# Kernel optimization log

Hardware: AMD Instinct MI355X
Metric: run time of the kernel (lower is better)

## Reference

```python
import jax, jax.numpy as jnp
import numpy as np

D_MODEL = 1024
NUM_HEADS = 16
D_K = D_MODEL // NUM_HEADS
THETA = 10000.0
BATCH = 4
SEQ = 2048


def rope(x, positions, theta=THETA):
    # x: [B, H, S, d_k]; rotate interleaved pairs (x_{2i}, x_{2i+1})
    d_k = x.shape[-1]
    inv_freq = theta ** (-jnp.arange(0, d_k, 2, dtype=jnp.float32) / d_k)  # [d_k/2]
    ang = positions[:, None].astype(jnp.float32) * inv_freq[None, :]  # [S, d_k/2]
    cos, sin = jnp.cos(ang), jnp.sin(ang)
    x1 = x[..., 0::2]
    x2 = x[..., 1::2]
    r1 = x1 * cos - x2 * sin
    r2 = x1 * sin + x2 * cos
    out = jnp.stack([r1, r2], axis=-1).reshape(x.shape)
    return out.astype(x.dtype)


def setup_inputs() -> dict:
    key = jax.random.key(0)
    k0, k1, k2, k3, k4 = jax.random.split(key, 5)
    std_qk = 2.0 / (D_MODEL + D_MODEL)
    x = jax.random.normal(k0, (BATCH, SEQ, D_MODEL), dtype=jnp.float32)
    P_Q = jax.random.normal(k1, (D_MODEL, D_MODEL), dtype=jnp.float32) * std_qk
    P_K = jax.random.normal(k2, (D_MODEL, D_MODEL), dtype=jnp.float32) * std_qk
    P_V = jax.random.normal(k3, (D_MODEL, D_MODEL), dtype=jnp.float32) * std_qk
    P_O = jax.random.normal(k4, (D_MODEL, D_MODEL), dtype=jnp.float32) * std_qk
    return {"x": x, "P_Q": P_Q, "P_K": P_K, "P_V": P_V, "P_O": P_O}


def reference(x, P_Q, P_K, P_V, P_O):
    B, S, _ = x.shape
    positions = jnp.arange(S)

    def proj(P):
        y = jnp.einsum('bsd,ed->bse', x, P)  # e = num_heads*d_k
        return y.reshape(B, S, NUM_HEADS, D_K).transpose(0, 2, 1, 3)  # [B,H,S,d_k]

    Q = rope(proj(P_Q), positions)
    K = rope(proj(P_K), positions)
    V = proj(P_V)

    scores = jnp.einsum('bhqd,bhkd->bhqk', Q, K) / jnp.sqrt(jnp.asarray(D_K, x.dtype))
    causal = jnp.tril(jnp.ones((S, S), dtype=bool))
    scores = jnp.where(causal, scores, jnp.asarray(-jnp.inf, scores.dtype))
    attn = jax.nn.softmax(scores, axis=-1)
    out = jnp.einsum('bhqk,bhkd->bhqd', attn, V)  # [B,H,S,d_v]
    out = out.transpose(0, 2, 1, 3).reshape(B, S, NUM_HEADS * D_K)
    return jnp.einsum('bse,de->bsd', out, P_O)
```

## Files before the change

kernel.cpp:

```cpp
#include <hip/hip_runtime.h>

typedef unsigned short u16;
typedef unsigned int u32;
typedef float f32x4 __attribute__((ext_vector_type(4)));
typedef __bf16 bf16x8 __attribute__((ext_vector_type(8)));

#define S_LEN 2048
#define DMODEL 1024
#define NHEAD 16
#define DKH 64

__device__ __forceinline__ u16 f2bf(float f) {
    unsigned u = __float_as_uint(f);
    u += 0x7FFFu + ((u >> 16) & 1u);
    return (u16)(u >> 16);
}
__device__ __forceinline__ u32 pk2(float a, float b) {
    return (u32)f2bf(a) | ((u32)f2bf(b) << 16);
}

__device__ __forceinline__ void glds16(const u16* g, u16* l) {
    __builtin_amdgcn_global_load_lds(
        (const __attribute__((address_space(1))) void*)(g),
        (__attribute__((address_space(3))) void*)(l), 16, 0, 0);
}

__global__ __launch_bounds__(256) void cvt_kernel(const float* __restrict__ in,
                                                  u16* __restrict__ out, int n4) {
    int i = blockIdx.x * 256 + threadIdx.x;
    if (i >= n4) return;
    float4 v = reinterpret_cast<const float4*>(in)[i];
    uint2 o;
    o.x = (unsigned)f2bf(v.x) | ((unsigned)f2bf(v.y) << 16);
    o.y = (unsigned)f2bf(v.z) | ((unsigned)f2bf(v.w) << 16);
    reinterpret_cast<uint2*>(out)[i] = o;
}

__device__ __forceinline__ void gemm_core(const u16* __restrict__ A, const u16* __restrict__ Bt,
                                          int K, int m0, int n0,
                                          u16* As, u16* Bs, f32x4 acc[4][4]) {
    const int tid  = threadIdx.x;
    const int lane = tid & 63;
    const int quad = lane >> 4, l15 = lane & 15;
    const int w    = tid >> 6;
    const int mq   = w & 1, nq = w >> 1;

    const int c0 = tid, c1 = tid + 256;
    const int r0 = c0 >> 2, k0 = ((c0 & 3) ^ (r0 & 3)) * 8;
    const int r1 = c1 >> 2, k1 = ((c1 & 3) ^ (r1 & 3)) * 8;
    const u16* ga0 = A  + (size_t)(m0 + r0) * K + k0;
    const u16* ga1 = A  + (size_t)(m0 + r1) * K + k1;
    const u16* gb0 = Bt + (size_t)(n0 + r0) * K + k0;
    const u16* gb1 = Bt + (size_t)(n0 + r1) * K + k1;
    u16* la0 = As + c0 * 8; u16* la1 = As + c1 * 8;
    u16* lb0 = Bs + c0 * 8; u16* lb1 = Bs + c1 * 8;

    const int swz = (quad ^ (l15 & 3)) * 8;
    const u16* ra = As + (mq * 64 + l15) * 32 + swz;
    const u16* rb = Bs + (nq * 64 + l15) * 32 + swz;

    for (int kk = 0; kk < K; kk += 32) {
        __syncthreads();
        glds16(ga0 + kk, la0);
        glds16(ga1 + kk, la1);
        glds16(gb0 + kk, lb0);
        glds16(gb1 + kk, lb1);
        __syncthreads();
        bf16x8 af[4], bfv[4];
#pragma unroll
        for (int t = 0; t < 4; ++t) {
            af[t]  = *reinterpret_cast<const bf16x8*>(ra + t * 512);
            bfv[t] = *reinterpret_cast<const bf16x8*>(rb + t * 512);
        }
#pragma unroll
        for (int mt = 0; mt < 4; ++mt)
#pragma unroll
            for (int nt = 0; nt < 4; ++nt)
                acc[mt][nt] = __builtin_amdgcn_mfma_f32_16x16x32_bf16(af[mt], bfv[nt], acc[mt][nt], 0, 0, 0);
    }
}

__global__ __launch_bounds__(256) void gemm_qkv_kernel(const u16* __restrict__ xb, const u16* __restrict__ Wqkv,
                                                       u16* __restrict__ Qb, u16* __restrict__ Kb,
                                                       u16* __restrict__ Vt) {
    __shared__ u16 As[128 * 32];
    __shared__ u16 Bs[128 * 32];
    f32x4 acc[4][4];
    const f32x4 zz = {0.f, 0.f, 0.f, 0.f};
#pragma unroll
    for (int i = 0; i < 4; ++i)
#pragma unroll
        for (int j = 0; j < 4; ++j) acc[i][j] = zz;

    const int m0 = blockIdx.y * 128;
    const int n0 = blockIdx.x * 128;
    gemm_core(xb, Wqkv, DMODEL, m0, n0, As, Bs, acc);

    const int lane = threadIdx.x & 63;
    const int quad = lane >> 4, l15 = lane & 15;
    const int w = threadIdx.x >> 6, mq = w & 1, nq = w >> 1;

#pragma unroll
    for (int nt = 0; nt < 4; ++nt) {
        const int ncol = n0 + nq*64 + nt*16 + l15;
        const int sel  = ncol >> 10;
        const int e    = ncol & 1023;
        const int h    = e >> 6, dk = e & 63;
#pragma unroll
        for (int mt = 0; mt < 4; ++mt) {
            const int mrow = m0 + mq*64 + mt*16 + quad*4;
            if (sel == 2) {
#pragma unroll
                for (int r = 0; r < 4; ++r) {
                    int m = mrow + r;
                    int b = m >> 11, s = m & 2047;
                    Vt[((size_t)(b * NHEAD + h) * DKH + dk) * S_LEN + s] = f2bf(acc[mt][nt][r]);
                }
            } else {
                float invf = exp2f(-13.2877124f * (float)(dk & 62) * (1.0f / 64.0f));
                u16* dst = sel ? Kb : Qb;
#pragma unroll
                for (int r = 0; r < 4; ++r) {
                    float val  = acc[mt][nt][r];
                    float part = __shfl_xor(val, 1);
                    int m = mrow + r;
                    int b = m >> 11, s = m & 2047;
                    float ang = (float)s * invf;
                    float sn, cs;
                    __sincosf(ang, &sn, &cs);
                    float o = (dk & 1) ? (part * sn + val * cs)
                                       : (val * cs - part * sn);
                    dst[((size_t)(b * NHEAD + h) * S_LEN + s) * DKH + dk] = f2bf(o);
                }
            }
        }
    }
}

__global__ __launch_bounds__(256) void attn_kernel(const u16* __restrict__ Qb, const u16* __restrict__ Kb,
                                                   const u16* __restrict__ Vt, u16* __restrict__ A2) {
    __shared__ u16 Ks[64 * 64];
    __shared__ u16 Vs[64 * 64];
    __shared__ u16 Ps[4][32 * 64];

    const int tid  = threadIdx.x;
    const int lane = tid & 63, w = tid >> 6;
    const int quad = lane >> 4, l15 = lane & 15;
    const int bh   = blockIdx.x & 63;
    const int qb   = 15 - (blockIdx.x >> 6);
    const int b = bh >> 4, h = bh & 15;
    const int q0w = qb * 128 + w * 32;
    const int nkt = 2 * (qb + 1);
    const int sw7 = l15 & 7;
    const float csc = 0.125f * 1.44269504f;
    const f32x4 zz = {0.f, 0.f, 0.f, 0.f};

    bf16x8 qf[2][2];
#pragma unroll
    for (int qt2 = 0; qt2 < 2; ++qt2)
#pragma unroll
        for (int hh = 0; hh < 2; ++hh)
            qf[qt2][hh] = *reinterpret_cast<const bf16x8*>(
                Qb + ((size_t)bh * S_LEN + q0w + qt2 * 16 + l15) * DKH + hh * 32 + quad * 8);

    f32x4 st[4][2], ot[4][2];
#pragma unroll
    for (int mt = 0; mt < 4; ++mt) { ot[mt][0] = zz; ot[mt][1] = zz; }
    float mi[2] = {-3.0e38f, -3.0e38f}, li[2] = {0.f, 0.f};

    const int c0 = tid, c1 = tid + 256;
    const int r0 = c0 >> 3, kc0 = ((c0 & 7) ^ (r0 & 7)) * 8;
    const int r1 = c1 >> 3, kc1 = ((c1 & 7) ^ (r1 & 7)) * 8;
    const u16* gk0 = Kb + ((size_t)bh * S_LEN + r0) * DKH + kc0;
    const u16* gk1 = Kb + ((size_t)bh * S_LEN + r1) * DKH + kc1;
    const u16* gv0 = Vt + ((size_t)bh * DKH + r0) * S_LEN + kc0;
    const u16* gv1 = Vt + ((size_t)bh * DKH + r1) * S_LEN + kc1;
    u16* lk0 = Ks + c0 * 8; u16* lk1 = Ks + c1 * 8;
    u16* lv0 = Vs + c0 * 8; u16* lv1 = Vs + c1 * 8;
    u16* Pw = &Ps[w][0];

    for (int kt = 0; kt < nkt; ++kt) {
        const int key0 = kt * 64;
        __syncthreads();
        glds16(gk0 + (size_t)key0 * DKH, lk0);
        glds16(gk1 + (size_t)key0 * DKH, lk1);
        glds16(gv0 + key0, lv0);
        glds16(gv1 + key0, lv1);
        __syncthreads();

#pragma unroll
        for (int kt4 = 0; kt4 < 4; ++kt4) {
            const u16* krow = Ks + (kt4 * 16 + l15) * 64;
            bf16x8 ka0 = *reinterpret_cast<const bf16x8*>(krow + (quad ^ sw7) * 8);
            bf16x8 ka1 = *reinterpret_cast<const bf16x8*>(krow + ((4 + quad) ^ sw7) * 8);
#pragma unroll
            for (int qt2 = 0; qt2 < 2; ++qt2) {
                f32x4 s = __builtin_amdgcn_mfma_f32_16x16x32_bf16(ka0, qf[qt2][0], zz, 0, 0, 0);
                st[kt4][qt2] = __builtin_amdgcn_mfma_f32_16x16x32_bf16(ka1, qf[qt2][1], s, 0, 0, 0);
            }
        }

        if (key0 + 63 > q0w) {
#pragma unroll
            for (int qt2 = 0; qt2 < 2; ++qt2) {
                const int qrow = q0w + qt2 * 16 + l15;
#pragma unroll
                for (int kt4 = 0; kt4 < 4; ++kt4) {
                    const int kbase = key0 + kt4 * 16 + quad * 4;
#pragma unroll
                    for (int r = 0; r < 4; ++r)
                        if (kbase + r > qrow) st[kt4][qt2][r] = -3.0e38f;
                }
            }
        }

#pragma unroll
        for (int qt2 = 0; qt2 < 2; ++qt2) {
            float rm = st[0][qt2][0];
#pragma unroll
            for (int kt4 = 0; kt4 < 4; ++kt4)
#pragma unroll
                for (int r = 0; r < 4; ++r) rm = fmaxf(rm, st[kt4][qt2][r]);
            rm = fmaxf(rm, __shfl_xor(rm, 16));
            rm = fmaxf(rm, __shfl_xor(rm, 32));
            const float mn = fmaxf(mi[qt2], rm);
            const float al = exp2f((mi[qt2] - mn) * csc);
            mi[qt2] = mn;
            const float nb = mn * csc;
            float rs = 0.f;
#pragma unroll
            for (int kt4 = 0; kt4 < 4; ++kt4)
#pragma unroll
                for (int r = 0; r < 4; ++r) {
                    float p = exp2f(st[kt4][qt2][r] * csc - nb);
                    st[kt4][qt2][r] = p;
                    rs += p;
                }
            rs += __shfl_xor(rs, 16);
            rs += __shfl_xor(rs, 32);
            li[qt2] = li[qt2] * al + rs;
#pragma unroll
            for (int mt = 0; mt < 4; ++mt)
#pragma unroll
                for (int r = 0; r < 4; ++r) ot[mt][qt2][r] *= al;

            u16* prow = Pw + (qt2 * 16 + l15) * 64 + (quad & 1) * 4;
#pragma unroll
            for (int kt4 = 0; kt4 < 4; ++kt4) {
                uint2 pv;
                pv.x = pk2(st[kt4][qt2][0], st[kt4][qt2][1]);
                pv.y = pk2(st[kt4][qt2][2], st[kt4][qt2][3]);
                *reinterpret_cast<uint2*>(prow + ((2 * kt4 + (quad >> 1)) ^ sw7) * 8) = pv;
            }
        }
        __threadfence_block();

        bf16x8 pb[2][2];
#pragma unroll
        for (int qt2 = 0; qt2 < 2; ++qt2)
#pragma unroll
            for (int kh = 0; kh < 2; ++kh)
                pb[qt2][kh] = *reinterpret_cast<const bf16x8*>(
                    Pw + (qt2 * 16 + l15) * 64 + ((kh * 4 + quad) ^ sw7) * 8);
#pragma unroll
        for (int mt = 0; mt < 4; ++mt) {
            const u16* vrow = Vs + (mt * 16 + l15) * 64;
            bf16x8 va0 = *reinterpret_cast<const bf16x8*>(vrow + (quad ^ sw7) * 8);
            bf16x8 va1 = *reinterpret_cast<const bf16x8*>(vrow + ((4 + quad) ^ sw7) * 8);
#pragma unroll
            for (int qt2 = 0; qt2 < 2; ++qt2) {
                ot[mt][qt2] = __builtin_amdgcn_mfma_f32_16x16x32_bf16(va0, pb[qt2][0], ot[mt][qt2], 0, 0, 0);
                ot[mt][qt2] = __builtin_amdgcn_mfma_f32_16x16x32_bf16(va1, pb[qt2][1], ot[mt][qt2], 0, 0, 0);
            }
        }
    }

#pragma unroll
    for (int qt2 = 0; qt2 < 2; ++qt2) {
        const float il = 1.0f / li[qt2];
        u16* prow = Pw + (qt2 * 16 + l15) * 64 + (quad & 1) * 4;
#pragma unroll
        for (int mt = 0; mt < 4; ++mt) {
            uint2 ov;
            ov.x = pk2(ot[mt][qt2][0] * il, ot[mt][qt2][1] * il);
            ov.y = pk2(ot[mt][qt2][2] * il, ot[mt][qt2][3] * il);
            *reinterpret_cast<uint2*>(prow + ((2 * mt + (quad >> 1)) ^ sw7) * 8) = ov;
        }
    }
    __threadfence_block();
    const int r2 = lane >> 1, half = lane & 1;
    const u16* orow = Pw + r2 * 64;
    u16* gout = A2 + ((size_t)b * S_LEN + q0w + r2) * DMODEL + h * DKH + half * 32;
#pragma unroll
    for (int c = 0; c < 4; ++c) {
        uint4 val = *reinterpret_cast<const uint4*>(orow + (((half * 4 + c) ^ (r2 & 7))) * 8);
        *reinterpret_cast<uint4*>(gout + c * 8) = val;
    }
}

__global__ __launch_bounds__(256) void gemm_oproj_kernel(const u16* __restrict__ A2, const u16* __restrict__ Wo,
                                                         float* __restrict__ Cout) {
    __shared__ u16 As[128 * 32];
    __shared__ u16 Bs[128 * 32];
    f32x4 acc[4][4];
    const f32x4 zz = {0.f, 0.f, 0.f, 0.f};
#pragma unroll
    for (int i = 0; i < 4; ++i)
#pragma unroll
        for (int j = 0; j < 4; ++j) acc[i][j] = zz;

    const int m0 = blockIdx.y * 128;
    const int n0 = blockIdx.x * 128;
    gemm_core(A2, Wo, DMODEL, m0, n0, As, Bs, acc);

    const int lane = threadIdx.x & 63;
    const int quad = lane >> 4, l15 = lane & 15;
    const int w = threadIdx.x >> 6, mq = w & 1, nq = w >> 1;
#pragma unroll
    for (int nt = 0; nt < 4; ++nt) {
        const int ncol = n0 + nq*64 + nt*16 + l15;
#pragma unroll
        for (int mt = 0; mt < 4; ++mt) {
            const int mrow = m0 + mq*64 + mt*16 + quad*4;
#pragma unroll
            for (int r = 0; r < 4; ++r)
                Cout[(size_t)(mrow + r) * DMODEL + ncol] = acc[mt][nt][r];
        }
    }
}

extern "C" void kernel_launch(void* const* d_in, const int* in_sizes, int n_in,
                              void* d_out, int out_size, void* d_ws, size_t ws_size,
                              hipStream_t stream) {
    const float* x  = (const float*)d_in[0];
    const float* PQ = (const float*)d_in[1];
    const float* PK = (const float*)d_in[2];
    const float* PV = (const float*)d_in[3];
    const float* PO = (const float*)d_in[4];
    float* out = (float*)d_out;
    char* ws = (char*)d_ws;

    const size_t MB = 1u << 20;
    u16* xb   = (u16*)(ws + 0 * MB);
    u16* Wqkv = (u16*)(ws + 16 * MB);
    u16* Wo   = (u16*)(ws + 22 * MB);
    u16* Qb   = (u16*)(ws + 24 * MB);
    u16* Kb   = (u16*)(ws + 40 * MB);
    u16* Vt   = (u16*)(ws + 56 * MB);
    u16* A2   = (u16*)(ws + 72 * MB);

    cvt_kernel<<<dim3(8192), dim3(256), 0, stream>>>(x,  xb,            2097152);
    cvt_kernel<<<dim3(1024), dim3(256), 0, stream>>>(PQ, Wqkv,           262144);
    cvt_kernel<<<dim3(1024), dim3(256), 0, stream>>>(PK, Wqkv + 1048576, 262144);
    cvt_kernel<<<dim3(1024), dim3(256), 0, stream>>>(PV, Wqkv + 2097152, 262144);
    cvt_kernel<<<dim3(1024), dim3(256), 0, stream>>>(PO, Wo,             262144);

    gemm_qkv_kernel<<<dim3(24, 64), dim3(256), 0, stream>>>(xb, Wqkv, Qb, Kb, Vt);

    attn_kernel<<<dim3(1024), dim3(256), 0, stream>>>(Qb, Kb, Vt, A2);

    gemm_oproj_kernel<<<dim3(8, 64), dim3(256), 0, stream>>>(A2, Wo, out);
}
```

Measured before the change: 314.3 us.

## Double-buffer K/V tiles, pair causal query blocks, and cheapen softmax/RoPE math

The attention kernel now double-buffers the K/V shared-memory tiles and issues the next tile's async load before computing on the current one, so global loads overlap with MFMA work. Each workgroup processes a short and a long causal query block in turn, which balances work across the halved grid. The online softmax skips the rescale of the output accumulator when no row maximum grew, bf16 packing uses the hardware packed-convert builtin, and RoPE uses range-reduced native sin/cos. These trade extra LDS and some rounding and sin/cos accuracy differences for less load latency and fewer ALU instructions.

```diff
diff --git a/kernel.cpp b/kernel.cpp
--- a/kernel.cpp
+++ b/kernel.cpp
@@ -15,8 +15,15 @@
     u += 0x7FFFu + ((u >> 16) & 1u);
     return (u16)(u >> 16);
 }
-__device__ __forceinline__ u32 pk2(float a, float b) {
+
+__device__ __forceinline__ u32 pkbf2(float a, float b) {
+#if __has_builtin(__builtin_amdgcn_cvt_pk_bf16_f32)
+    typedef __bf16 bf16x2_t __attribute__((ext_vector_type(2)));
+    bf16x2_t r = __builtin_amdgcn_cvt_pk_bf16_f32(a, b);
+    u32 u; __builtin_memcpy(&u, &r, 4); return u;
+#else
     return (u32)f2bf(a) | ((u32)f2bf(b) << 16);
+#endif
 }
 
 __device__ __forceinline__ void glds16(const u16* g, u16* l) {
@@ -117,7 +124,7 @@
                     Vt[((size_t)(b * NHEAD + h) * DKH + dk) * S_LEN + s] = f2bf(acc[mt][nt][r]);
                 }
             } else {
-                float invf = exp2f(-13.2877124f * (float)(dk & 62) * (1.0f / 64.0f));
+                float invf_rev = 0.15915494f * exp2f(-13.2877124f * (float)(dk & 62) * (1.0f / 64.0f));
                 u16* dst = sel ? Kb : Qb;
 #pragma unroll
                 for (int r = 0; r < 4; ++r) {
@@ -125,9 +132,15 @@
                     float part = __shfl_xor(val, 1);
                     int m = mrow + r;
                     int b = m >> 11, s = m & 2047;
-                    float ang = (float)s * invf;
+                    float rev = (float)s * invf_rev;
+                    float fr  = rev - floorf(rev);
+#if __has_builtin(__builtin_amdgcn_sinf) && __has_builtin(__builtin_amdgcn_cosf)
+                    float sn = __builtin_amdgcn_sinf(fr);
+                    float cs = __builtin_amdgcn_cosf(fr);
+#else
                     float sn, cs;
-                    __sincosf(ang, &sn, &cs);
+                    __sincosf(fr * 6.2831853f, &sn, &cs);
+#endif
                     float o = (dk & 1) ? (part * sn + val * cs)
                                        : (val * cs - part * sn);
                     dst[((size_t)(b * NHEAD + h) * S_LEN + s) * DKH + dk] = f2bf(o);
@@ -139,34 +152,19 @@
 
 __global__ __launch_bounds__(256) void attn_kernel(const u16* __restrict__ Qb, const u16* __restrict__ Kb,
                                                    const u16* __restrict__ Vt, u16* __restrict__ A2) {
-    __shared__ u16 Ks[64 * 64];
-    __shared__ u16 Vs[64 * 64];
+    __shared__ u16 Ks[2][64 * 64];
+    __shared__ u16 Vs[2][64 * 64];
     __shared__ u16 Ps[4][32 * 64];
 
     const int tid  = threadIdx.x;
     const int lane = tid & 63, w = tid >> 6;
     const int quad = lane >> 4, l15 = lane & 15;
     const int bh   = blockIdx.x & 63;
-    const int qb   = 15 - (blockIdx.x >> 6);
+    const int pr   = blockIdx.x >> 6;
     const int b = bh >> 4, h = bh & 15;
-    const int q0w = qb * 128 + w * 32;
-    const int nkt = 2 * (qb + 1);
     const int sw7 = l15 & 7;
     const float csc = 0.125f * 1.44269504f;
     const f32x4 zz = {0.f, 0.f, 0.f, 0.f};
-
-    bf16x8 qf[2][2];
-#pragma unroll
-    for (int qt2 = 0; qt2 < 2; ++qt2)
-#pragma unroll
-        for (int hh = 0; hh < 2; ++hh)
-            qf[qt2][hh] = *reinterpret_cast<const bf16x8*>(
-                Qb + ((size_t)bh * S_LEN + q0w + qt2 * 16 + l15) * DKH + hh * 32 + quad * 8);
-
-    f32x4 st[4][2], ot[4][2];
-#pragma unroll
-    for (int mt = 0; mt < 4; ++mt) { ot[mt][0] = zz; ot[mt][1] = zz; }
-    float mi[2] = {-3.0e38f, -3.0e38f}, li[2] = {0.f, 0.f};
 
     const int c0 = tid, c1 = tid + 256;
     const int r0 = c0 >> 3, kc0 = ((c0 & 7) ^ (r0 & 7)) * 8;
@@ -175,126 +173,159 @@
     const u16* gk1 = Kb + ((size_t)bh * S_LEN + r1) * DKH + kc1;
     const u16* gv0 = Vt + ((size_t)bh * DKH + r0) * S_LEN + kc0;
     const u16* gv1 = Vt + ((size_t)bh * DKH + r1) * S_LEN + kc1;
-    u16* lk0 = Ks + c0 * 8; u16* lk1 = Ks + c1 * 8;
-    u16* lv0 = Vs + c0 * 8; u16* lv1 = Vs + c1 * 8;
     u16* Pw = &Ps[w][0];
 
-    for (int kt = 0; kt < nkt; ++kt) {
-        const int key0 = kt * 64;
+#pragma unroll 1
+    for (int ph = 0; ph < 2; ++ph) {
+        const int qb  = ph ? (15 - pr) : pr;
+        const int q0w = qb * 128 + w * 32;
+        const int nkt = 2 * (qb + 1);
+
+        bf16x8 qf[2][2];
+#pragma unroll
+        for (int qt2 = 0; qt2 < 2; ++qt2)
+#pragma unroll
+            for (int hh = 0; hh < 2; ++hh)
+                qf[qt2][hh] = *reinterpret_cast<const bf16x8*>(
+                    Qb + ((size_t)bh * S_LEN + q0w + qt2 * 16 + l15) * DKH + hh * 32 + quad * 8);
+
+        f32x4 st[4][2], ot[4][2];
+#pragma unroll
+        for (int mt = 0; mt < 4; ++mt) { ot[mt][0] = zz; ot[mt][1] = zz; }
+        float mi[2] = {-3.0e38f, -3.0e38f}, li[2] = {0.f, 0.f};
+
         __syncthreads();
-        glds16(gk0 + (size_t)key0 * DKH, lk0);
-        glds16(gk1 + (size_t)key0 * DKH, lk1);
-        glds16(gv0 + key0, lv0);
-        glds16(gv1 + key0, lv1);
-        __syncthreads();
-
-#pragma unroll
-        for (int kt4 = 0; kt4 < 4; ++kt4) {
-            const u16* krow = Ks + (kt4 * 16 + l15) * 64;
-            bf16x8 ka0 = *reinterpret_cast<const bf16x8*>(krow + (quad ^ sw7) * 8);
-            bf16x8 ka1 = *reinterpret_cast<const bf16x8*>(krow + ((4 + quad) ^ sw7) * 8);
+        glds16(gk0, &Ks[0][0] + c0 * 8);
+        glds16(gk1, &Ks[0][0] + c1 * 8);
+        glds16(gv0, &Vs[0][0] + c0 * 8);
+        glds16(gv1, &Vs[0][0] + c1 * 8);
+
+#pragma unroll 1
+        for (int kt = 0; kt < nkt; ++kt) {
+            const int key0 = kt * 64;
+            __syncthreads();
+            if (kt + 1 < nkt) {
+                const int nx = (kt + 1) & 1;
+                const size_t nkey = (size_t)(key0 + 64);
+                glds16(gk0 + nkey * DKH, &Ks[nx][0] + c0 * 8);
+                glds16(gk1 + nkey * DKH, &Ks[nx][0] + c1 * 8);
+                glds16(gv0 + nkey, &Vs[nx][0] + c0 * 8);
+                glds16(gv1 + nkey, &Vs[nx][0] + c1 * 8);
+            }
+            const u16* Kbuf = &Ks[kt & 1][0];
+            const u16* Vbuf = &Vs[kt & 1][0];
+
+#pragma unroll
+            for (int kt4 = 0; kt4 < 4; ++kt4) {
+                const u16* krow = Kbuf + (kt4 * 16 + l15) * 64;
+                bf16x8 ka0 = *reinterpret_cast<const bf16x8*>(krow + (quad ^ sw7) * 8);
+                bf16x8 ka1 = *reinterpret_cast<const bf16x8*>(krow + ((4 + quad) ^ sw7) * 8);
+#pragma unroll
+                for (int qt2 = 0; qt2 < 2; ++qt2) {
+                    f32x4 s = __builtin_amdgcn_mfma_f32_16x16x32_bf16(ka0, qf[qt2][0], zz, 0, 0, 0);
+                    st[kt4][qt2] = __builtin_amdgcn_mfma_f32_16x16x32_bf16(ka1, qf[qt2][1], s, 0, 0, 0);
+                }
+            }
+
+            if (key0 + 63 > q0w) {
+#pragma unroll
+                for (int qt2 = 0; qt2 < 2; ++qt2) {
+                    const int qrow = q0w + qt2 * 16 + l15;
+#pragma unroll
+                    for (int kt4 = 0; kt4 < 4; ++kt4) {
+                        const int kbase = key0 + kt4 * 16 + quad * 4;
+#pragma unroll
+                        for (int r = 0; r < 4; ++r)
+                            if (kbase + r > qrow) st[kt4][qt2][r] = -3.0e38f;
+                    }
+                }
+            }
+
 #pragma unroll
             for (int qt2 = 0; qt2 < 2; ++qt2) {
-                f32x4 s = __builtin_amdgcn_mfma_f32_16x16x32_bf16(ka0, qf[qt2][0], zz, 0, 0, 0);
-                st[kt4][qt2] = __builtin_amdgcn_mfma_f32_16x16x32_bf16(ka1, qf[qt2][1], s, 0, 0, 0);
-            }
-        }
-
-        if (key0 + 63 > q0w) {
-#pragma unroll
-            for (int qt2 = 0; qt2 < 2; ++qt2) {
-                const int qrow = q0w + qt2 * 16 + l15;
+                float rm = st[0][qt2][0];
+#pragma unroll
+                for (int kt4 = 0; kt4 < 4; ++kt4)
+#pragma unroll
+                    for (int r = 0; r < 4; ++r) rm = fmaxf(rm, st[kt4][qt2][r]);
+                rm = fmaxf(rm, __shfl_xor(rm, 16));
+                rm = fmaxf(rm, __shfl_xor(rm, 32));
+                if (__ballot(rm > mi[qt2])) {
+                    const float mn = fmaxf(mi[qt2], rm);
+                    const float al = exp2f((mi[qt2] - mn) * csc);
+                    mi[qt2] = mn;
+                    li[qt2] *= al;
+#pragma unroll
+                    for (int mt = 0; mt < 4; ++mt)
+#pragma unroll
+                        for (int r = 0; r < 4; ++r) ot[mt][qt2][r] *= al;
+                }
+                const float nb = mi[qt2] * csc;
+                float rs = 0.f;
+#pragma unroll
+                for (int kt4 = 0; kt4 < 4; ++kt4)
+#pragma unroll
+                    for (int r = 0; r < 4; ++r) {
+                        float p = exp2f(st[kt4][qt2][r] * csc - nb);
+                        st[kt4][qt2][r] = p;
+                        rs += p;
+                    }
+                rs += __shfl_xor(rs, 16);
+                rs += __shfl_xor(rs, 32);
+                li[qt2] += rs;
+
+                u16* prow = Pw + (qt2 * 16 + l15) * 64 + (quad & 1) * 4;
 #pragma unroll
                 for (int kt4 = 0; kt4 < 4; ++kt4) {
-                    const int kbase = key0 + kt4 * 16 + quad * 4;
-#pragma unroll
-                    for (int r = 0; r < 4; ++r)
-                        if (kbase + r > qrow) st[kt4][qt2][r] = -3.0e38f;
+                    uint2 pv;
+                    pv.x = pkbf2(st[kt4][qt2][0], st[kt4][qt2][1]);
+                    pv.y = pkbf2(st[kt4][qt2][2], st[kt4][qt2][3]);
+                    *reinterpret_cast<uint2*>(prow + ((2 * kt4 + (quad >> 1)) ^ sw7) * 8) = pv;
+                }
+            }
+            __threadfence_block();
+
+            bf16x8 pb[2][2];
+#pragma unroll
+            for (int qt2 = 0; qt2 < 2; ++qt2)
+#pragma unroll
+                for (int kh = 0; kh < 2; ++kh)
+                    pb[qt2][kh] = *reinterpret_cast<const bf16x8*>(
+                        Pw + (qt2 * 16 + l15) * 64 + ((kh * 4 + quad) ^ sw7) * 8);
+#pragma unroll
+            for (int mt = 0; mt < 4; ++mt) {
+                const u16* vrow = Vbuf + (mt * 16 + l15) * 64;
+                bf16x8 va0 = *reinterpret_cast<const bf16x8*>(vrow + (quad ^ sw7) * 8);
+                bf16x8 va1 = *reinterpret_cast<const bf16x8*>(vrow + ((4 + quad) ^ sw7) * 8);
+#pragma unroll
+                for (int qt2 = 0; qt2 < 2; ++qt2) {
+                    ot[mt][qt2] = __builtin_amdgcn_mfma_f32_16x16x32_bf16(va0, pb[qt2][0], ot[mt][qt2], 0, 0, 0);
+                    ot[mt][qt2] = __builtin_amdgcn_mfma_f32_16x16x32_bf16(va1, pb[qt2][1], ot[mt][qt2], 0, 0, 0);
                 }
             }
         }
 
 #pragma unroll
         for (int qt2 = 0; qt2 < 2; ++qt2) {
-            float rm = st[0][qt2][0];
-#pragma unroll
-            for (int kt4 = 0; kt4 < 4; ++kt4)
-#pragma unroll
-                for (int r = 0; r < 4; ++r) rm = fmaxf(rm, st[kt4][qt2][r]);
-            rm = fmaxf(rm, __shfl_xor(rm, 16));
-            rm = fmaxf(rm, __shfl_xor(rm, 32));
-            const float mn = fmaxf(mi[qt2], rm);
-            const float al = exp2f((mi[qt2] - mn) * csc);
-            mi[qt2] = mn;
-            const float nb = mn * csc;
-            float rs = 0.f;
-#pragma unroll
-            for (int kt4 = 0; kt4 < 4; ++kt4)
-#pragma unroll
-                for (int r = 0; r < 4; ++r) {
-                    float p = exp2f(st[kt4][qt2][r] * csc - nb);
-                    st[kt4][qt2][r] = p;
-                    rs += p;
-                }
-            rs += __shfl_xor(rs, 16);
-            rs += __shfl_xor(rs, 32);
-            li[qt2] = li[qt2] * al + rs;
-#pragma unroll
-            for (int mt = 0; mt < 4; ++mt)
-#pragma unroll
-                for (int r = 0; r < 4; ++r) ot[mt][qt2][r] *= al;
-
+            const float il = 1.0f / li[qt2];
             u16* prow = Pw + (qt2 * 16 + l15) * 64 + (quad & 1) * 4;
 #pragma unroll
-            for (int kt4 = 0; kt4 < 4; ++kt4) {
-                uint2 pv;
-                pv.x = pk2(st[kt4][qt2][0], st[kt4][qt2][1]);
-                pv.y = pk2(st[kt4][qt2][2], st[kt4][qt2][3]);
-                *reinterpret_cast<uint2*>(prow + ((2 * kt4 + (quad >> 1)) ^ sw7) * 8) = pv;
+            for (int mt = 0; mt < 4; ++mt) {
+                uint2 ov;
+                ov.x = pkbf2(ot[mt][qt2][0] * il, ot[mt][qt2][1] * il);
+                ov.y = pkbf2(ot[mt][qt2][2] * il, ot[mt][qt2][3] * il);
+                *reinterpret_cast<uint2*>(prow + ((2 * mt + (quad >> 1)) ^ sw7) * 8) = ov;
             }
         }
         __threadfence_block();
-
-        bf16x8 pb[2][2];
-#pragma unroll
-        for (int qt2 = 0; qt2 < 2; ++qt2)
-#pragma unroll
-            for (int kh = 0; kh < 2; ++kh)
-                pb[qt2][kh] = *reinterpret_cast<const bf16x8*>(
-                    Pw + (qt2 * 16 + l15) * 64 + ((kh * 4 + quad) ^ sw7) * 8);
-#pragma unroll
-        for (int mt = 0; mt < 4; ++mt) {
-            const u16* vrow = Vs + (mt * 16 + l15) * 64;
-            bf16x8 va0 = *reinterpret_cast<const bf16x8*>(vrow + (quad ^ sw7) * 8);
-            bf16x8 va1 = *reinterpret_cast<const bf16x8*>(vrow + ((4 + quad) ^ sw7) * 8);
-#pragma unroll
-            for (int qt2 = 0; qt2 < 2; ++qt2) {
-                ot[mt][qt2] = __builtin_amdgcn_mfma_f32_16x16x32_bf16(va0, pb[qt2][0], ot[mt][qt2], 0, 0, 0);
-                ot[mt][qt2] = __builtin_amdgcn_mfma_f32_16x16x32_bf16(va1, pb[qt2][1], ot[mt][qt2], 0, 0, 0);
-            }
-        }
-    }
-
-#pragma unroll
-    for (int qt2 = 0; qt2 < 2; ++qt2) {
-        const float il = 1.0f / li[qt2];
-        u16* prow = Pw + (qt2 * 16 + l15) * 64 + (quad & 1) * 4;
-#pragma unroll
-        for (int mt = 0; mt < 4; ++mt) {
-            uint2 ov;
-            ov.x = pk2(ot[mt][qt2][0] * il, ot[mt][qt2][1] * il);
-            ov.y = pk2(ot[mt][qt2][2] * il, ot[mt][qt2][3] * il);
-            *reinterpret_cast<uint2*>(prow + ((2 * mt + (quad >> 1)) ^ sw7) * 8) = ov;
-        }
-    }
-    __threadfence_block();
-    const int r2 = lane >> 1, half = lane & 1;
-    const u16* orow = Pw + r2 * 64;
-    u16* gout = A2 + ((size_t)b * S_LEN + q0w + r2) * DMODEL + h * DKH + half * 32;
-#pragma unroll
-    for (int c = 0; c < 4; ++c) {
-        uint4 val = *reinterpret_cast<const uint4*>(orow + (((half * 4 + c) ^ (r2 & 7))) * 8);
-        *reinterpret_cast<uint4*>(gout + c * 8) = val;
+        const int r2 = lane >> 1, half = lane & 1;
+        const u16* orow = Pw + r2 * 64;
+        u16* gout = A2 + ((size_t)b * S_LEN + q0w + r2) * DMODEL + h * DKH + half * 32;
+#pragma unroll
+        for (int c = 0; c < 4; ++c) {
+            uint4 val = *reinterpret_cast<const uint4*>(orow + (((half * 4 + c) ^ (r2 & 7))) * 8);
+            *reinterpret_cast<uint4*>(gout + c * 8) = val;
+        }
     }
 }
 
@@ -357,7 +388,7 @@
 
     gemm_qkv_kernel<<<dim3(24, 64), dim3(256), 0, stream>>>(xb, Wqkv, Qb, Kb, Vt);
 
-    attn_kernel<<<dim3(1024), dim3(256), 0, stream>>>(Qb, Kb, Vt, A2);
+    attn_kernel<<<dim3(512), dim3(256), 0, stream>>>(Qb, Kb, Vt, A2);
 
     gemm_oproj_kernel<<<dim3(8, 64), dim3(256), 0, stream>>>(A2, Wo, out);
 }
```

Result: no change. 315.1 us (+0.2%).
